# Performance work log

Measured on AMD Instinct MI355X. Metric: run time of the kernel, lower is better.

Reference implementation:

```python
import jax, jax.numpy as jnp
from jax import lax
import numpy as np

B, T, C, V, E, H, OC = 1024, 32, 14, 21128, 200, 50, 8


def gru(x, Wih, Whh, bih, bhh):
    # x: [N, T, E] -> hiddens [N, T, H]; torch nn.GRU gate order (r, z, n)
    Hd = Whh.shape[1]
    xp = jnp.einsum('nte,ge->ntg', x, Wih) + bih  # [N, T, 3H]
    h0 = jnp.zeros((x.shape[0], Hd), x.dtype)

    def step(h, xt):
        gh = h @ Whh.T + bhh
        r = jax.nn.sigmoid(xt[:, :Hd] + gh[:, :Hd])
        z = jax.nn.sigmoid(xt[:, Hd:2 * Hd] + gh[:, Hd:2 * Hd])
        n = jnp.tanh(xt[:, 2 * Hd:] + r * gh[:, 2 * Hd:])
        h_new = (1.0 - z) * n + z * h
        return h_new, h_new

    _, hs = lax.scan(step, h0, jnp.swapaxes(xp, 0, 1))
    return jnp.swapaxes(hs, 0, 1)


def setup_inputs():
    key = jax.random.key(0)
    ks = jax.random.split(key, 32)
    s = 0.1
    inp = {
        'contexts_indices': jax.random.randint(ks[0], (B, T), 0, V),
        'candidates_indices': jax.random.randint(ks[1], (B, C, T), 0, V),
        'y_dev': jax.random.uniform(ks[2], (B, C), dtype=jnp.float32),
        'emb': jax.random.normal(ks[3], (V, E), dtype=jnp.float32),
        'A': jax.random.normal(ks[4], (H, H), dtype=jnp.float32) * s,
        'Wih_c': jax.random.normal(ks[5], (3 * H, E), dtype=jnp.float32) * s,
        'Whh_c': jax.random.normal(ks[6], (3 * H, H), dtype=jnp.float32) * s,
        'bih_c': jnp.zeros((3 * H,), jnp.float32),
        'bhh_c': jnp.zeros((3 * H,), jnp.float32),
        'Wih_r': jax.random.normal(ks[7], (3 * H, E), dtype=jnp.float32) * s,
        'Whh_r': jax.random.normal(ks[8], (3 * H, H), dtype=jnp.float32) * s,
        'bih_r': jnp.zeros((3 * H,), jnp.float32),
        'bhh_r': jnp.zeros((3 * H,), jnp.float32),
        'conv_w': jax.random.normal(ks[9], (OC, 2, 3, 3), dtype=jnp.float32) * s,
        'Wih2': jax.random.normal(ks[10], (3 * H, OC * 10 * 10), dtype=jnp.float32) * s,
        'Whh2': jax.random.normal(ks[11], (3 * H, H), dtype=jnp.float32) * s,
        'bih2': jnp.zeros((3 * H,), jnp.float32),
        'bhh2': jnp.zeros((3 * H,), jnp.float32),
        'fc1_w': jax.random.normal(ks[12], (100, C * H), dtype=jnp.float32) * s,
        'fc1_b': jnp.zeros((100,), jnp.float32),
        'fc2_w': jax.random.normal(ks[13], (C, 100), dtype=jnp.float32) * s,
        'fc2_b': jnp.zeros((C,), jnp.float32),
    }
    return inp


def reference(contexts_indices, candidates_indices, y_dev, emb, A,
              Wih_c, Whh_c, bih_c, bhh_c, Wih_r, Whh_r, bih_r, bhh_r,
              conv_w, Wih2, Whh2, bih2, bhh2, fc1_w, fc1_b, fc2_w, fc2_b):
    b = contexts_indices.shape[0]
    ctx = contexts_indices[:, None, :]                      # [B,1,T]
    ctx_emb = emb[ctx]                                      # [B,1,T,E] (dropout = identity in eval)
    cand_emb = emb[candidates_indices]                      # [B,C,T,E]

    ctx_h = gru(ctx_emb.reshape(-1, T, E), Wih_c, Whh_c, bih_c, bhh_c).reshape(b, 1, T, H)
    cand_h = gru(cand_emb.reshape(-1, T, E), Wih_r, Whh_r, bih_r, bhh_r).reshape(b, C, T, H)

    M1 = jnp.einsum('btph,bcqh->btcpq', ctx_emb, cand_emb)  # [B,1,C,T,T]
    ctx_hA = jnp.einsum('btij,jk->btik', ctx_h, A)
    M2 = jnp.einsum('btph,bcqh->btcpq', ctx_hA, cand_h)

    # faithful to torch: stack on dim 2 then row-major view(-1, 2, T, T)
    M = jnp.stack([M1, M2], axis=2).reshape(-1, 2, T, T)    # [B*C, 2, T, T]

    conv = lax.conv_general_dilated(M, conv_w, (1, 1), 'VALID',
                                    dimension_numbers=('NCHW', 'OIHW', 'NCHW'))  # [B*C, OC, 30, 30]
    pooled = lax.reduce_window(conv, -jnp.inf, lax.max,
                               (1, 1, 3, 3), (1, 1, 3, 3), 'VALID')              # [B*C, OC, 10, 10]

    feats = pooled.reshape(b, C, OC * 10 * 10)              # [B, C, 800]
    Hs = gru(feats, Wih2, Whh2, bih2, bhh2)                 # [B, C, H]
    flat = Hs.reshape(b, -1)                                # [B, C*H]

    hid = jax.nn.relu(flat @ fc1_w.T + fc1_b)
    log_probs = jax.nn.log_softmax(hid @ fc2_w.T + fc2_b, axis=-1)  # softmax then log
    kl = jnp.where(y_dev > 0, y_dev * (jnp.log(y_dev) - log_probs), 0.0)
    return jnp.mean(kl)
```

## Files before the change

kernel.cpp:

```cpp
#include <hip/hip_runtime.h>
#include <math.h>

typedef unsigned short u16;
typedef short s16;
typedef u16 u16x8 __attribute__((ext_vector_type(8)));
typedef s16 short8v __attribute__((ext_vector_type(8)));
typedef float f32x4 __attribute__((ext_vector_type(4)));

__device__ __forceinline__ float b2f(u16 u) {
    return __uint_as_float(((unsigned)u) << 16);
}
__device__ __forceinline__ u16 f2b(float f) {
    unsigned u = __float_as_uint(f);
    unsigned r = (u + 0x7FFFu + ((u >> 16) & 1u)) >> 16;
    return (u16)r;
}

__global__ __launch_bounds__(256) void k_cvt4(
    const float* __restrict__ s0, u16* __restrict__ d0, long n0,
    const float* __restrict__ s1, u16* __restrict__ d1, long n1,
    const float* __restrict__ s2, u16* __restrict__ d2, long n2,
    const float* __restrict__ s3, u16* __restrict__ d3, long n3)
{
    long j = (long)blockIdx.x * 256 + threadIdx.x;
    const float* s; u16* d;
    if (j < n0) { s = s0; d = d0; }
    else {
        j -= n0;
        if (j < n1) { s = s1; d = d1; }
        else {
            j -= n1;
            if (j < n2) { s = s2; d = d2; }
            else {
                j -= n2;
                if (j < n3) { s = s3; d = d3; }
                else return;
            }
        }
    }
    float4 v = ((const float4*)s)[j];
    *(ushort4*)(d + j * 4) = make_ushort4(f2b(v.x), f2b(v.y), f2b(v.z), f2b(v.w));
}

__global__ __launch_bounds__(256) void k_projmm2(
    const u16* __restrict__ embh, const u16* __restrict__ wc,
    const u16* __restrict__ wr, const float* __restrict__ bc,
    const float* __restrict__ br, u16* __restrict__ outc,
    u16* __restrict__ outr, int V)
{
    __shared__ s16 Ab[2048];
    __shared__ s16 Bb[2560];
    __shared__ float bhL[160];
    const int t = threadIdx.x;
    const int w = t >> 6, l = t & 63, lg = l >> 4, lr = l & 15;
    int id = blockIdx.x;
    const int half = (id >= 662) ? 1 : 0;
    id -= half * 662;
    const u16* wh = half ? wr : wc;
    const float* bias = half ? br : bc;
    u16* outp = half ? outr : outc;
    const int mb = id >> 1, nb = id & 1;
    const long rowbase = (long)mb * 64;
    const int colbase = nb * 80;
    if (t < 160) bhL[t] = (t < 150) ? bias[t] : 0.f;

    f32x4 acc[5];
#pragma unroll
    for (int i = 0; i < 5; ++i) acc[i] = (f32x4){0,0,0,0};

    for (int ch = 0; ch < 7; ++ch) {
        __syncthreads();
        {
            int kc = t >> 6, row = t & 63;
            long grow = rowbase + row; if (grow >= V) grow = V - 1;
            int k0 = ch * 32 + kc * 8;
            short8v v = {0,0,0,0,0,0,0,0};
            if (k0 < 200) v = *(const short8v*)(embh + grow * 200 + k0);
            *(short8v*)&Ab[t * 8] = v;
        }
        for (int it = t; it < 320; it += 256) {
            int kc = it / 80, col = it % 80;
            int gcol = colbase + col;
            int k0 = ch * 32 + kc * 8;
            short8v v = {0,0,0,0,0,0,0,0};
            if (gcol < 150 && k0 < 200)
                v = *(const short8v*)(wh + (size_t)gcol * 200 + k0);
            *(short8v*)&Bb[it * 8] = v;
        }
        __syncthreads();
        short8v a = *(short8v*)&Ab[(lg * 64 + w * 16 + lr) * 8];
#pragma unroll
        for (int ct = 0; ct < 5; ++ct) {
            short8v bv = *(short8v*)&Bb[(lg * 80 + ct * 16 + lr) * 8];
            acc[ct] = __builtin_amdgcn_mfma_f32_16x16x32_bf16(a, bv, acc[ct], 0, 0, 0);
        }
    }
#pragma unroll
    for (int ct = 0; ct < 5; ++ct) {
        int gcol = colbase + ct * 16 + lr;
        if (gcol < 150) {
#pragma unroll
            for (int rr = 0; rr < 4; ++rr) {
                long row = rowbase + w * 16 + lg * 4 + rr;
                outp[row * 152 + gcol] = f2b(acc[ct][rr] + bhL[gcol]);
            }
        }
    }
}

template<int MODE, int SEQS>
__device__ __forceinline__ void gru_body(
    const void* __restrict__ xp_, const int* __restrict__ idx,
    const float* __restrict__ Whh, const float* __restrict__ bhh,
    void* __restrict__ hs_, int T, long blk)
{
    __shared__ s16  hbuf[1024];
    __shared__ float ghL[SEQS * 160];
    __shared__ float hL[SEQS * 52];
    __shared__ float bhL[152];
    __shared__ u16 xraw[4864];
    const int t = threadIdx.x;
    const int w = t >> 6, l = t & 63, lg = l >> 4, lr = l & 15;
    constexpr int HST = (MODE == 2) ? 56 : 50;
    constexpr int XROW = SEQS * 152;
    u16*   xbH = xraw;
    float* xbF = (float*)xraw;

    for (int li = t; li < 1024; li += 256) hbuf[li] = 0;
    for (int e = t; e < SEQS * 52; e += 256) hL[e] = 0.f;
    if (t < 152) bhL[t] = (t < 150) ? bhh[t] : 0.f;

    const int te_0 = (w * 3     > 9) ? 9 : w * 3;
    const int te_1 = (w * 3 + 1 > 9) ? 9 : w * 3 + 1;
    const int te_2 = (w * 3 + 2 > 9) ? 9 : w * 3 + 2;
    short8v B00 = {0,0,0,0,0,0,0,0}, B01 = B00, B10 = B00, B11 = B00, B20 = B00, B21 = B00;
    {
        int cols[3] = { te_0 * 16 + lr, te_1 * 16 + lr, te_2 * 16 + lr };
        short8v* frg[6] = { &B00, &B01, &B10, &B11, &B20, &B21 };
#pragma unroll
        for (int ti = 0; ti < 3; ++ti) {
            int col = cols[ti];
            if (col < 150) {
#pragma unroll
                for (int s = 0; s < 2; ++s) {
                    short8v v = {0,0,0,0,0,0,0,0};
#pragma unroll
                    for (int e = 0; e < 8; ++e) {
                        int k = (s * 4 + lg) * 8 + e;
                        if (k < 50) v[e] = (s16)f2b(Whh[col * 50 + k]);
                    }
                    *frg[ti * 2 + s] = v;
                }
            }
        }
    }

    const long seqbase = blk * SEQS;
    const float* xpf = (const float*)xp_;
    const u16*   xph = (const u16*)xp_;
    float* hsf = (float*)hs_;
    u16*   hsh = (u16*)hs_;

    const int rA = (MODE == 2) ? t / 19 : t / 38;
    const int oA = (MODE == 2) ? (t % 19) * 8 : (t % 38) * 4;
    const int rB = (MODE == 2) ? (t + 256) / 19 : (t + 256) / 38;
    const int oB = (MODE == 2) ? ((t + 256) % 19) * 8 : ((t + 256) % 38) * 4;
    const bool actA = (MODE == 2) ? (t < SEQS * 19) : true;
    const bool hasB = (MODE == 2) ? (t + 256 < SEQS * 19) : (t + 256 < SEQS * 38);

    auto rowbase = [&](int rr, int stp) -> size_t {
        long r = seqbase + rr;
        long src = (MODE == 0) ? (r * T + stp) : (long)idx[r * T + stp];
        return (size_t)src * 152;
    };

    if (MODE == 2) {
        if (actA) *(u16x8*)&xbH[rA * 152 + oA] = *(const u16x8*)(xph + rowbase(rA, 0) + oA);
        if (hasB) *(u16x8*)&xbH[rB * 152 + oB] = *(const u16x8*)(xph + rowbase(rB, 0) + oB);
    } else {
        *(float4*)&xbF[rA * 152 + oA] = *(const float4*)(xpf + rowbase(rA, 0) + oA);
        if (hasB)
            *(float4*)&xbF[rB * 152 + oB] = *(const float4*)(xpf + rowbase(rB, 0) + oB);
    }
    __syncthreads();

    for (int st = 0; st < T; ++st) {
        const int cur = st & 1;
        u16x8 pfh0, pfh1;
        float4 pf0, pf1;
        if (st + 1 < T) {
            if (MODE == 2) {
                if (actA) pfh0 = *(const u16x8*)(xph + rowbase(rA, st + 1) + oA);
                if (hasB) pfh1 = *(const u16x8*)(xph + rowbase(rB, st + 1) + oB);
            } else {
                pf0 = *(const float4*)(xpf + rowbase(rA, st + 1) + oA);
                if (hasB) pf1 = *(const float4*)(xpf + rowbase(rB, st + 1) + oB);
            }
        }
        short8v a0 = *(short8v*)&hbuf[((0 + lg) * 16 + lr) * 8];
        short8v a1 = *(short8v*)&hbuf[((4 + lg) * 16 + lr) * 8];
        f32x4 c0 = {0,0,0,0}, c1 = {0,0,0,0}, c2 = {0,0,0,0};
        c0 = __builtin_amdgcn_mfma_f32_16x16x32_bf16(a0, B00, c0, 0, 0, 0);
        c0 = __builtin_amdgcn_mfma_f32_16x16x32_bf16(a1, B01, c0, 0, 0, 0);
        c1 = __builtin_amdgcn_mfma_f32_16x16x32_bf16(a0, B10, c1, 0, 0, 0);
        c1 = __builtin_amdgcn_mfma_f32_16x16x32_bf16(a1, B11, c1, 0, 0, 0);
        c2 = __builtin_amdgcn_mfma_f32_16x16x32_bf16(a0, B20, c2, 0, 0, 0);
        c2 = __builtin_amdgcn_mfma_f32_16x16x32_bf16(a1, B21, c2, 0, 0, 0);
        if (lg * 4 < SEQS) {
            int col0 = te_0 * 16 + lr, col1 = te_1 * 16 + lr, col2 = te_2 * 16 + lr;
            if (col0 < 150) {
#pragma unroll
                for (int r = 0; r < 4; ++r) ghL[(lg * 4 + r) * 160 + col0] = c0[r] + bhL[col0];
            }
            if (col1 < 150) {
#pragma unroll
                for (int r = 0; r < 4; ++r) ghL[(lg * 4 + r) * 160 + col1] = c1[r] + bhL[col1];
            }
            if (col2 < 150) {
#pragma unroll
                for (int r = 0; r < 4; ++r) ghL[(lg * 4 + r) * 160 + col2] = c2[r] + bhL[col2];
            }
        }
        __syncthreads();
        if (st + 1 < T) {
            if (MODE == 2) {
                if (actA) *(u16x8*)&xbH[(cur ^ 1) * XROW + rA * 152 + oA] = pfh0;
                if (hasB) *(u16x8*)&xbH[(cur ^ 1) * XROW + rB * 152 + oB] = pfh1;
            } else {
                *(float4*)&xbF[(cur ^ 1) * XROW + rA * 152 + oA] = pf0;
                if (hasB) *(float4*)&xbF[(cur ^ 1) * XROW + rB * 152 + oB] = pf1;
            }
        }
        for (int item = t; item < SEQS * 50; item += 256) {
            int ss = item / 50, hh = item % 50;
            float xv0, xv1, xv2;
            if (MODE == 2) {
                const u16* xr = &xbH[cur * XROW + ss * 152];
                xv0 = b2f(xr[hh]); xv1 = b2f(xr[50 + hh]); xv2 = b2f(xr[100 + hh]);
            } else {
                const float* xr = &xbF[cur * XROW + ss * 152];
                xv0 = xr[hh]; xv1 = xr[50 + hh]; xv2 = xr[100 + hh];
            }
            float vr  = xv0 + ghL[ss * 160 + hh];
            float vz  = xv1 + ghL[ss * 160 + 50 + hh];
            float ghn = ghL[ss * 160 + 100 + hh];
            float rg = 1.f / (1.f + __expf(-vr));
            float zg = 1.f / (1.f + __expf(-vz));
            float a = xv2 + rg * ghn;
            a = fminf(fmaxf(a, -15.f), 15.f);
            float e2 = __expf(-2.f * a);
            float nn2 = (1.f - e2) / (1.f + e2);
            float hn = (1.f - zg) * nn2 + zg * hL[ss * 52 + hh];
            hL[ss * 52 + hh] = hn;
            hbuf[((hh >> 3) * 16 + ss) * 8 + (hh & 7)] = (s16)f2b(hn);
            size_t ofs = ((size_t)(seqbase + ss) * T + st) * HST + hh;
            if (MODE == 2) hsh[ofs] = f2b(hn); else hsf[ofs] = hn;
        }
        __syncthreads();
    }
}

__global__ __launch_bounds__(256) void k_scan_all(
    const u16* __restrict__ proj_ch, const u16* __restrict__ proj_rh,
    const int* __restrict__ ctx_idx, const int* __restrict__ cand_idx,
    const float* __restrict__ Whh_c, const float* __restrict__ Whh_r,
    const float* __restrict__ bhh_c, const float* __restrict__ bhh_r,
    u16* __restrict__ ctx_hh, u16* __restrict__ candh_h)
{
    const long bid = blockIdx.x;
    const bool cand = (bid < 896);
    gru_body<2, 16>(cand ? (const void*)proj_rh : (const void*)proj_ch,
                    cand ? cand_idx : ctx_idx,
                    cand ? Whh_r : Whh_c,
                    cand ? bhh_r : bhh_c,
                    cand ? (void*)candh_h : (void*)ctx_hh,
                    32, cand ? bid : bid - 896);
}

__global__ __launch_bounds__(256) void k_scan2(
    const float* __restrict__ xp2, const float* __restrict__ Whh2,
    const float* __restrict__ bhh2, float* __restrict__ hs2)
{
    gru_body<0, 8>(xp2, nullptr, Whh2, bhh2, hs2, 14, (long)blockIdx.x);
}

__global__ __launch_bounds__(256) void k_matA(
    const u16* __restrict__ inh, const float* __restrict__ A,
    u16* __restrict__ outh)
{
    __shared__ float AL[50 * 52];
    __shared__ float inL[32 * 52];
    const int t = threadIdx.x;
    for (int e = t; e < 2500; e += 256) AL[(e / 50) * 52 + (e % 50)] = A[e];
    const long rbase = (long)blockIdx.x * 32;
    for (int e = t; e < 1600; e += 256) {
        int r = e / 50, j = e % 50;
        inL[r * 52 + j] = b2f(inh[(rbase + r) * 56 + j]);
    }
    __syncthreads();
    for (int item = t; item < 1600; item += 256) {
        int r = item / 50, kk = item % 50;
        float acc = 0.f;
#pragma unroll 10
        for (int j = 0; j < 50; ++j)
            acc += inL[r * 52 + j] * AL[j * 52 + kk];
        outh[(rbase + r) * 56 + kk] = f2b(acc);
    }
}

__global__ __launch_bounds__(256) void k_matchconv(
    const u16* __restrict__ embh, const int* __restrict__ ctx_idx,
    const int* __restrict__ cand_idx, const u16* __restrict__ ctxA_h,
    const u16* __restrict__ candh_h, const float* __restrict__ conv_w,
    u16* __restrict__ feats, int b0)
{
    __shared__ s16 pool16[9480];
    __shared__ float wL[144];
    __shared__ int ci[32], qi[2][32];
    u16* Mb    = (u16*)pool16;
    u16* convL = (u16*)pool16 + 2184;
    const int t = threadIdx.x;
    const int wg = blockIdx.x;
    const int xcd = wg & 7, q = wg >> 3;
    const int r = q % 14, bq = q / 14;
    const int b = b0 + bq * 8 + xcd;
    const long nl = (long)(bq * 8 + xcd) * 14 + r;
    const int w = t >> 6, l = t & 63, lg = l >> 4, lr = l & 15;

    if (t < 144) wL[t] = conv_w[t];

    f32x4 cacc0 = {0,0,0,0}, cacc1 = {0,0,0,0};
    const int job0 = w * 2, job1 = w * 2 + 1;
    const int ch0 = job0 >> 2, rt0 = (job0 >> 1) & 1, ct0 = job0 & 1;
    const int ch1 = job1 >> 2, rt1 = (job1 >> 1) & 1, ct1 = job1 & 1;

    if (r < 7) {
        const int c0 = 2 * r;
        if (t < 32) ci[t] = ctx_idx[b * 32 + t];
        else if (t < 96)
            qi[(t - 32) >> 5][t & 31] =
                cand_idx[((long)b * 14 + c0 + ((t - 32) >> 5)) * 32 + (t & 31)];
        __syncthreads();
        s16* ctxL = pool16;
        s16* canL = pool16 + 3168;
#pragma unroll
        for (int cnk = 0; cnk < 3; ++cnk) {
            const int kcbase = (cnk == 0) ? 0 : (cnk == 1 ? 12 : 20);
            const int kccnt  = (cnk == 0) ? 12 : 8;
            const int scnt   = (cnk == 0) ? 3 : 2;
            if (cnk) __syncthreads();
            for (int it = t; it < kccnt * 32; it += 256) {
                int kcl = it >> 5, row = it & 31;
                int kc = kcbase + kcl;
                short8v v = {0,0,0,0,0,0,0,0};
                if (kc < 25) v = *(const short8v*)(embh + (size_t)ci[row] * 200 + kc * 8);
                *(short8v*)&ctxL[(kcl * 33 + row) * 8] = v;
            }
            for (int it = t; it < kccnt * 64; it += 256) {
                int kcl = it >> 6, col = it & 63;
                int kc = kcbase + kcl;
                short8v v = {0,0,0,0,0,0,0,0};
                if (kc < 25)
                    v = *(const short8v*)(embh + (size_t)qi[col >> 5][col & 31] * 200 + kc * 8);
                *(short8v*)&canL[(kcl * 65 + col) * 8] = v;
            }
            __syncthreads();
            for (int sl = 0; sl < scnt; ++sl) {
                int kcl = sl * 4 + lg;
                short8v a0 = *(short8v*)&ctxL[(kcl * 33 + rt0 * 16 + lr) * 8];
                short8v b0 = *(short8v*)&canL[(kcl * 65 + ch0 * 32 + ct0 * 16 + lr) * 8];
                short8v b1 = *(short8v*)&canL[(kcl * 65 + ch1 * 32 + ct1 * 16 + lr) * 8];
                cacc0 = __builtin_amdgcn_mfma_f32_16x16x32_bf16(a0, b0, cacc0, 0, 0, 0);
                short8v a1 = (rt0 == rt1) ? a0
                           : *(short8v*)&ctxL[(kcl * 33 + rt1 * 16 + lr) * 8];
                cacc1 = __builtin_amdgcn_mfma_f32_16x16x32_bf16(a1, b1, cacc1, 0, 0, 0);
            }
        }
    } else {
        const int c0 = 2 * (r - 7);
        s16* aL = pool16;
        s16* cL = pool16 + 2112;
        for (int it = t; it < 256; it += 256) {
            int kc = it >> 5, row = it & 31;
            short8v v = {0,0,0,0,0,0,0,0};
            if (kc < 7) {
                v = *(const short8v*)(ctxA_h + (size_t)(b * 32 + row) * 56 + kc * 8);
                if (kc == 6) { v[2] = 0; v[3] = 0; v[4] = 0; v[5] = 0; v[6] = 0; v[7] = 0; }
            }
            *(short8v*)&aL[(kc * 33 + row) * 8] = v;
        }
        for (int it = t; it < 512; it += 256) {
            int kc = it >> 6, col = it & 63;
            long row = ((long)(b - b0) * 14 + c0 + (col >> 5)) * 32 + (col & 31);
            short8v v = {0,0,0,0,0,0,0,0};
            if (kc < 7) {
                v = *(const short8v*)(candh_h + (size_t)row * 56 + kc * 8);
                if (kc == 6) { v[2] = 0; v[3] = 0; v[4] = 0; v[5] = 0; v[6] = 0; v[7] = 0; }
            }
            *(short8v*)&cL[(kc * 65 + col) * 8] = v;
        }
        __syncthreads();
#pragma unroll
        for (int sl = 0; sl < 2; ++sl) {
            int kcl = sl * 4 + lg;
            short8v a0 = *(short8v*)&aL[(kcl * 33 + rt0 * 16 + lr) * 8];
            short8v b0 = *(short8v*)&cL[(kcl * 65 + ch0 * 32 + ct0 * 16 + lr) * 8];
            short8v b1 = *(short8v*)&cL[(kcl * 65 + ch1 * 32 + ct1 * 16 + lr) * 8];
            cacc0 = __builtin_amdgcn_mfma_f32_16x16x32_bf16(a0, b0, cacc0, 0, 0, 0);
            short8v a1 = (rt0 == rt1) ? a0
                       : *(short8v*)&aL[(kcl * 33 + rt1 * 16 + lr) * 8];
            cacc1 = __builtin_amdgcn_mfma_f32_16x16x32_bf16(a1, b1, cacc1, 0, 0, 0);
        }
    }

    __syncthreads();
#pragma unroll
    for (int rr = 0; rr < 4; ++rr) {
        Mb[ch0 * 1092 + (rt0 * 16 + lg * 4 + rr) * 33 + ct0 * 16 + lr] = f2b(cacc0[rr]);
        Mb[ch1 * 1092 + (rt1 * 16 + lg * 4 + rr) * 33 + ct1 * 16 + lr] = f2b(cacc1[rr]);
    }

    short8v Bc = {0,0,0,0,0,0,0,0};
    int dlt[8];
#pragma unroll
    for (int e = 0; e < 8; ++e) {
        int s = lg * 8 + e;
        if (s < 18) {
            int ch = s / 9, r9 = s % 9, ky = r9 / 3, kx = r9 % 3;
            dlt[e] = ch * 1092 + ky * 33 + kx;
            if (lr < 8) Bc[e] = (s16)f2b(wL[lr * 18 + s]);
        } else dlt[e] = 0;
    }
    __syncthreads();

    for (int tile = w; tile < 57; tile += 4) {
        int m = tile * 16 + lr;
        int cy = m / 30, cx = m - cy * 30;
        int base = cy * 33 + cx;
        short8v a;
#pragma unroll
        for (int e = 0; e < 8; ++e) a[e] = (s16)Mb[base + dlt[e]];
        f32x4 c = {0,0,0,0};
        c = __builtin_amdgcn_mfma_f32_16x16x32_bf16(a, Bc, c, 0, 0, 0);
        if (lr < 8) {
#pragma unroll
            for (int rr = 0; rr < 4; ++rr)
                convL[(tile * 16 + lg * 4 + rr) * 8 + lr] = f2b(c[rr]);
        }
    }
    __syncthreads();

    for (int item = t; item < 800; item += 256) {
        int oc = item / 100, rem = item % 100, py = rem / 10, px = rem % 10;
        int m0 = (3 * py) * 30 + 3 * px;
        float mx = -1e30f;
#pragma unroll
        for (int dy = 0; dy < 3; ++dy)
#pragma unroll
            for (int dx = 0; dx < 3; ++dx)
                mx = fmaxf(mx, b2f(convL[(m0 + dy * 30 + dx) * 8 + oc]));
        feats[nl * 800 + item] = f2b(mx);
    }
}

__global__ __launch_bounds__(256) void k_xp2mm(
    const u16* __restrict__ feats, const u16* __restrict__ w2h,
    const float* __restrict__ bih2, float* __restrict__ out)
{
    __shared__ s16 Ab[2048];
    __shared__ s16 Bb[2560];
    __shared__ float bhL[160];
    const int t = threadIdx.x;
    const int w = t >> 6, l = t & 63, lg = l >> 4, lr = l & 15;
    const int mb = blockIdx.x >> 1, nb = blockIdx.x & 1;
    const long rowbase = (long)mb * 64;
    const int colbase = nb * 80;
    if (t < 160) bhL[t] = (t < 150) ? bih2[t] : 0.f;

    f32x4 acc[5];
#pragma unroll
    for (int i = 0; i < 5; ++i) acc[i] = (f32x4){0,0,0,0};

    for (int ch = 0; ch < 25; ++ch) {
        __syncthreads();
        {
            int kc = t >> 6, row = t & 63;
            *(short8v*)&Ab[t * 8] =
                *(const short8v*)(feats + (rowbase + row) * 800 + ch * 32 + kc * 8);
        }
        for (int it = t; it < 320; it += 256) {
            int kc = it / 80, col = it % 80;
            int gcol = colbase + col;
            short8v v = {0,0,0,0,0,0,0,0};
            if (gcol < 150)
                v = *(const short8v*)(w2h + (size_t)gcol * 800 + ch * 32 + kc * 8);
            *(short8v*)&Bb[it * 8] = v;
        }
        __syncthreads();
        short8v a = *(short8v*)&Ab[(lg * 64 + w * 16 + lr) * 8];
#pragma unroll
        for (int ct = 0; ct < 5; ++ct) {
            short8v bv = *(short8v*)&Bb[(lg * 80 + ct * 16 + lr) * 8];
            acc[ct] = __builtin_amdgcn_mfma_f32_16x16x32_bf16(a, bv, acc[ct], 0, 0, 0);
        }
    }
#pragma unroll
    for (int ct = 0; ct < 5; ++ct) {
        int gcol = colbase + ct * 16 + lr;
        if (gcol < 150) {
#pragma unroll
            for (int rr = 0; rr < 4; ++rr) {
                long row = rowbase + w * 16 + lg * 4 + rr;
                out[row * 152 + gcol] = acc[ct][rr] + bhL[gcol];
            }
        }
    }
}

__global__ __launch_bounds__(128) void k_head(
    const float* __restrict__ Hs, const float* __restrict__ w1,
    const float* __restrict__ b1, const float* __restrict__ w2,
    const float* __restrict__ b2, const float* __restrict__ y,
    float* __restrict__ partial)
{
    __shared__ float hr[700];
    __shared__ float hidL[100];
    const int t = threadIdx.x;
    const long b = blockIdx.x;
    for (int e = t; e < 700; e += 128) hr[e] = Hs[b * 700 + e];
    __syncthreads();
    if (t < 100) {
        float acc = b1[t];
        const float4* wp = (const float4*)(w1 + (size_t)t * 700);
        for (int k4 = 0; k4 < 175; ++k4) {
            float4 wv = wp[k4];
            float4 hv = *(float4*)&hr[k4 * 4];
            acc += wv.x * hv.x + wv.y * hv.y + wv.z * hv.z + wv.w * hv.w;
        }
        hidL[t] = fmaxf(acc, 0.f);
    }
    __syncthreads();
    if (t < 64) {
        float logit = -1e30f;
        if (t < 14) {
            logit = b2[t];
            for (int k = 0; k < 100; ++k) logit += hidL[k] * w2[t * 100 + k];
        }
        float m = logit;
        for (int off = 8; off; off >>= 1) m = fmaxf(m, __shfl_xor(m, off, 16));
        float ex = (t < 14) ? __expf(logit - m) : 0.f;
        float se = ex;
        for (int off = 8; off; off >>= 1) se += __shfl_xor(se, off, 16);
        float kl = 0.f;
        if (t < 14) {
            float lp = logit - m - __logf(se);
            float yv = y[b * 14 + t];
            kl = (yv > 0.f) ? yv * (__logf(yv) - lp) : 0.f;
        }
        for (int off = 8; off; off >>= 1) kl += __shfl_xor(kl, off, 16);
        if (t == 0) partial[b] = kl;
    }
}

__global__ __launch_bounds__(256) void k_reduce(
    const float* __restrict__ partial, float* __restrict__ out)
{
    __shared__ float sm[256];
    const int t = threadIdx.x;
    sm[t] = partial[t] + partial[t + 256] + partial[t + 512] + partial[t + 768];
    __syncthreads();
    for (int off = 128; off; off >>= 1) {
        if (t < off) sm[t] += sm[t + off];
        __syncthreads();
    }
    if (t == 0) out[0] = sm[0] * (1.f / 14336.f);
}

extern "C" void kernel_launch(void* const* d_in, const int* in_sizes, int n_in,
                              void* d_out, int out_size, void* d_ws, size_t ws_size,
                              hipStream_t stream)
{
    const int*   ctx_idx  = (const int*)d_in[0];
    const int*   cand_idx = (const int*)d_in[1];
    const float* y_dev    = (const float*)d_in[2];
    const float* emb      = (const float*)d_in[3];
    const float* A        = (const float*)d_in[4];
    const float* Wih_c    = (const float*)d_in[5];
    const float* Whh_c    = (const float*)d_in[6];
    const float* bih_c    = (const float*)d_in[7];
    const float* bhh_c    = (const float*)d_in[8];
    const float* Wih_r    = (const float*)d_in[9];
    const float* Whh_r    = (const float*)d_in[10];
    const float* bih_r    = (const float*)d_in[11];
    const float* bhh_r    = (const float*)d_in[12];
    const float* conv_w   = (const float*)d_in[13];
    const float* Wih2     = (const float*)d_in[14];
    const float* Whh2     = (const float*)d_in[15];
    const float* bih2     = (const float*)d_in[16];
    const float* bhh2     = (const float*)d_in[17];
    const float* fc1_w    = (const float*)d_in[18];
    const float* fc1_b    = (const float*)d_in[19];
    const float* fc2_w    = (const float*)d_in[20];
    const float* fc2_b    = (const float*)d_in[21];

    float* ws = (float*)d_ws;
    u16*   embh    = (u16*)ws;
    u16*   proj_ch = (u16*)(ws + 2112800);
    u16*   proj_rh = (u16*)(ws + 3722784);
    u16*   ctx_hh  = (u16*)(ws + 5332768);
    u16*   ctxA_h  = (u16*)(ws + 6250272);
    u16*   candh_h = (u16*)(ws + 7167776);
    u16*   feats_h = (u16*)(ws + 20012832);
    u16*   w2h     = (u16*)(ws + 25747232);
    u16*   wch     = (u16*)(ws + 25807232);
    u16*   wrh     = (u16*)(ws + 25822232);
    float* xp2     = ws + 25837232;
    float* hs2     = ws + 28016304;
    float* part    = ws + 28733104;

    k_cvt4 <<<4303, 256, 0, stream>>>(emb, embh, 1056400,
                                      Wih2, w2h, 30000,
                                      Wih_c, wch, 7500,
                                      Wih_r, wrh, 7500);
    k_projmm2 <<<1324, 256, 0, stream>>>(embh, wch, wrh, bih_c, bih_r,
                                         proj_ch, proj_rh, 21128);
    k_scan_all <<<960, 256, 0, stream>>>(proj_ch, proj_rh, ctx_idx, cand_idx,
                                         Whh_c, Whh_r, bhh_c, bhh_r,
                                         ctx_hh, candh_h);
    k_matA <<<1024, 256, 0, stream>>>(ctx_hh, A, ctxA_h);
    k_matchconv <<<14336, 256, 0, stream>>>(embh, ctx_idx, cand_idx, ctxA_h, candh_h,
                                            conv_w, feats_h, 0);
    k_xp2mm <<<448, 256, 0, stream>>>(feats_h, w2h, bih2, xp2);
    k_scan2 <<<128, 256, 0, stream>>>(xp2, Whh2, bhh2, hs2);
    k_head <<<1024, 128, 0, stream>>>(hs2, fc1_w, fc1_b, fc2_w, fc2_b, y_dev, part);
    k_reduce <<<1, 256, 0, stream>>>(part, (float*)d_out);
}
```

Before: 330.6 us.

## Run M1 match-conv blocks alongside GRU scans and transpose feats layout

The M1 half of the match/conv work depends only on embeddings, so its blocks now run in the same launch as the context/candidate GRU scans. That fills the GPU while the 960 latency-bound scan blocks execute. The M2 half becomes its own kernel after matA. The pooled features are now stored position-major with 8 channels contiguous, written as vectorized 16-byte stores, and Wih2 is permuted during conversion to match. The mixed kernel carries the larger shared-memory footprint of the scan code for every block, which may lower occupancy for the M1 blocks.

Result: faster. 303.9 us (-8.1%).

```diff
diff --git a/kernel.cpp b/kernel.cpp
--- a/kernel.cpp
+++ b/kernel.cpp
@@ -16,30 +16,36 @@
     return (u16)r;
 }
 
-__global__ __launch_bounds__(256) void k_cvt4(
-    const float* __restrict__ s0, u16* __restrict__ d0, long n0,
-    const float* __restrict__ s1, u16* __restrict__ d1, long n1,
-    const float* __restrict__ s2, u16* __restrict__ d2, long n2,
-    const float* __restrict__ s3, u16* __restrict__ d3, long n3)
+__global__ __launch_bounds__(256) void k_cvt_all(
+    const float* __restrict__ emb, u16* __restrict__ embh,
+    const float* __restrict__ wcf, u16* __restrict__ wch,
+    const float* __restrict__ wrf, u16* __restrict__ wrh,
+    const float* __restrict__ w2f, u16* __restrict__ w2h)
 {
     long j = (long)blockIdx.x * 256 + threadIdx.x;
-    const float* s; u16* d;
-    if (j < n0) { s = s0; d = d0; }
-    else {
-        j -= n0;
-        if (j < n1) { s = s1; d = d1; }
-        else {
-            j -= n1;
-            if (j < n2) { s = s2; d = d2; }
-            else {
-                j -= n2;
-                if (j < n3) { s = s3; d = d3; }
-                else return;
-            }
-        }
-    }
-    float4 v = ((const float4*)s)[j];
-    *(ushort4*)(d + j * 4) = make_ushort4(f2b(v.x), f2b(v.y), f2b(v.z), f2b(v.w));
+    if (j < 1056400) {
+        float4 v = ((const float4*)emb)[j];
+        *(ushort4*)(embh + j * 4) = make_ushort4(f2b(v.x), f2b(v.y), f2b(v.z), f2b(v.w));
+        return;
+    }
+    j -= 1056400;
+    if (j < 7500) {
+        float4 v = ((const float4*)wcf)[j];
+        *(ushort4*)(wch + j * 4) = make_ushort4(f2b(v.x), f2b(v.y), f2b(v.z), f2b(v.w));
+        return;
+    }
+    j -= 7500;
+    if (j < 7500) {
+        float4 v = ((const float4*)wrf)[j];
+        *(ushort4*)(wrh + j * 4) = make_ushort4(f2b(v.x), f2b(v.y), f2b(v.z), f2b(v.w));
+        return;
+    }
+    j -= 7500;
+    if (j < 120000) {
+        int jj = (int)(j / 800), k = (int)(j % 800);
+        int p = k >> 3, oc = k & 7;
+        w2h[jj * 800 + k] = f2b(w2f[jj * 800 + oc * 100 + p]);
+    }
 }
 
 __global__ __launch_bounds__(256) void k_projmm2(
@@ -110,15 +116,15 @@
 
 template<int MODE, int SEQS>
 __device__ __forceinline__ void gru_body(
-    const void* __restrict__ xp_, const int* __restrict__ idx,
+    char* sm, const void* __restrict__ xp_, const int* __restrict__ idx,
     const float* __restrict__ Whh, const float* __restrict__ bhh,
     void* __restrict__ hs_, int T, long blk)
 {
-    __shared__ s16  hbuf[1024];
-    __shared__ float ghL[SEQS * 160];
-    __shared__ float hL[SEQS * 52];
-    __shared__ float bhL[152];
-    __shared__ u16 xraw[4864];
+    s16*   hbuf = (s16*)sm;
+    float* ghL  = (float*)(sm + 2048);
+    float* hL   = (float*)(sm + 2048 + SEQS * 640);
+    float* bhL  = (float*)(sm + 2048 + SEQS * 848);
+    u16*   xraw = (u16*)(sm + 2048 + SEQS * 848 + 608);
     const int t = threadIdx.x;
     const int w = t >> 6, l = t & 63, lg = l >> 4, lr = l & 15;
     constexpr int HST = (MODE == 2) ? 56 : 50;
@@ -260,28 +266,236 @@
     }
 }
 
-__global__ __launch_bounds__(256) void k_scan_all(
+__device__ __forceinline__ void conv_pool_epi(
+    char* sm, u16* __restrict__ feats, long nl, f32x4 cacc0, f32x4 cacc1)
+{
+    s16* pool16 = (s16*)sm;
+    float* wL = (float*)(sm + 18960);
+    u16* Mb    = (u16*)pool16;
+    u16* convL = (u16*)pool16 + 2184;
+    const int t = threadIdx.x;
+    const int w = t >> 6, l = t & 63, lg = l >> 4, lr = l & 15;
+    const int job0 = w * 2, job1 = w * 2 + 1;
+    const int ch0 = job0 >> 2, rt0 = (job0 >> 1) & 1, ct0 = job0 & 1;
+    const int ch1 = job1 >> 2, rt1 = (job1 >> 1) & 1, ct1 = job1 & 1;
+
+    __syncthreads();
+#pragma unroll
+    for (int rr = 0; rr < 4; ++rr) {
+        Mb[ch0 * 1092 + (rt0 * 16 + lg * 4 + rr) * 33 + ct0 * 16 + lr] = f2b(cacc0[rr]);
+        Mb[ch1 * 1092 + (rt1 * 16 + lg * 4 + rr) * 33 + ct1 * 16 + lr] = f2b(cacc1[rr]);
+    }
+
+    short8v Bc = {0,0,0,0,0,0,0,0};
+    int dlt[8];
+#pragma unroll
+    for (int e = 0; e < 8; ++e) {
+        int s = lg * 8 + e;
+        if (s < 18) {
+            int ch = s / 9, r9 = s % 9, ky = r9 / 3, kx = r9 % 3;
+            dlt[e] = ch * 1092 + ky * 33 + kx;
+            if (lr < 8) Bc[e] = (s16)f2b(wL[lr * 18 + s]);
+        } else dlt[e] = 0;
+    }
+    __syncthreads();
+
+    for (int tile = w; tile < 57; tile += 4) {
+        int m = tile * 16 + lr;
+        int cy = m / 30, cx = m - cy * 30;
+        int base = cy * 33 + cx;
+        short8v a;
+#pragma unroll
+        for (int e = 0; e < 8; ++e) a[e] = (s16)Mb[base + dlt[e]];
+        f32x4 c = {0,0,0,0};
+        c = __builtin_amdgcn_mfma_f32_16x16x32_bf16(a, Bc, c, 0, 0, 0);
+        if (lr < 8) {
+#pragma unroll
+            for (int rr = 0; rr < 4; ++rr)
+                convL[(tile * 16 + lg * 4 + rr) * 8 + lr] = f2b(c[rr]);
+        }
+    }
+    __syncthreads();
+
+    if (t < 100) {
+        int py = t / 10, px = t % 10;
+        int m0 = (3 * py) * 30 + 3 * px;
+        float mx[8];
+#pragma unroll
+        for (int c = 0; c < 8; ++c) mx[c] = -1e30f;
+#pragma unroll
+        for (int dy = 0; dy < 3; ++dy)
+#pragma unroll
+            for (int dx = 0; dx < 3; ++dx) {
+                u16x8 v = *(u16x8*)&convL[(m0 + dy * 30 + dx) * 8];
+#pragma unroll
+                for (int c = 0; c < 8; ++c) mx[c] = fmaxf(mx[c], b2f(v[c]));
+            }
+        u16x8 o;
+#pragma unroll
+        for (int c = 0; c < 8; ++c) o[c] = f2b(mx[c]);
+        *(u16x8*)(feats + nl * 800 + t * 8) = o;
+    }
+}
+
+__device__ __forceinline__ void m1_body(
+    char* sm, const u16* __restrict__ embh, const int* __restrict__ ctx_idx,
+    const int* __restrict__ cand_idx, const float* __restrict__ conv_w,
+    u16* __restrict__ feats, int wg)
+{
+    s16* pool16 = (s16*)sm;
+    float* wL = (float*)(sm + 18960);
+    int* ci = (int*)(sm + 19536);
+    int* qi = (int*)(sm + 19664);
+    const int t = threadIdx.x;
+    const int xcd = wg & 7, q = wg >> 3;
+    const int r = q % 7, bq = q / 7;
+    const int b = bq * 8 + xcd;
+    const long nl = (long)b * 14 + r;
+    const int w = t >> 6, l = t & 63, lg = l >> 4, lr = l & 15;
+
+    if (t < 144) wL[t] = conv_w[t];
+
+    f32x4 cacc0 = {0,0,0,0}, cacc1 = {0,0,0,0};
+    const int job0 = w * 2, job1 = w * 2 + 1;
+    const int ch0 = job0 >> 2, rt0 = (job0 >> 1) & 1, ct0 = job0 & 1;
+    const int ch1 = job1 >> 2, rt1 = (job1 >> 1) & 1, ct1 = job1 & 1;
+
+    const int c0 = 2 * r;
+    if (t < 32) ci[t] = ctx_idx[b * 32 + t];
+    else if (t < 96)
+        qi[((t - 32) >> 5) * 32 + (t & 31)] =
+            cand_idx[((long)b * 14 + c0 + ((t - 32) >> 5)) * 32 + (t & 31)];
+    __syncthreads();
+    s16* ctxL = pool16;
+    s16* canL = pool16 + 3168;
+#pragma unroll
+    for (int cnk = 0; cnk < 3; ++cnk) {
+        const int kcbase = (cnk == 0) ? 0 : (cnk == 1 ? 12 : 20);
+        const int kccnt  = (cnk == 0) ? 12 : 8;
+        const int scnt   = (cnk == 0) ? 3 : 2;
+        if (cnk) __syncthreads();
+        for (int it = t; it < kccnt * 32; it += 256) {
+            int kcl = it >> 5, row = it & 31;
+            int kc = kcbase + kcl;
+            short8v v = {0,0,0,0,0,0,0,0};
+            if (kc < 25) v = *(const short8v*)(embh + (size_t)ci[row] * 200 + kc * 8);
+            *(short8v*)&ctxL[(kcl * 33 + row) * 8] = v;
+        }
+        for (int it = t; it < kccnt * 64; it += 256) {
+            int kcl = it >> 6, col = it & 63;
+            int kc = kcbase + kcl;
+            short8v v = {0,0,0,0,0,0,0,0};
+            if (kc < 25)
+                v = *(const short8v*)(embh + (size_t)qi[(col >> 5) * 32 + (col & 31)] * 200 + kc * 8);
+            *(short8v*)&canL[(kcl * 65 + col) * 8] = v;
+        }
+        __syncthreads();
+        for (int sl = 0; sl < scnt; ++sl) {
+            int kcl = sl * 4 + lg;
+            short8v a0 = *(short8v*)&ctxL[(kcl * 33 + rt0 * 16 + lr) * 8];
+            short8v b0 = *(short8v*)&canL[(kcl * 65 + ch0 * 32 + ct0 * 16 + lr) * 8];
+            short8v b1 = *(short8v*)&canL[(kcl * 65 + ch1 * 32 + ct1 * 16 + lr) * 8];
+            cacc0 = __builtin_amdgcn_mfma_f32_16x16x32_bf16(a0, b0, cacc0, 0, 0, 0);
+            short8v a1 = (rt0 == rt1) ? a0
+                       : *(short8v*)&ctxL[(kcl * 33 + rt1 * 16 + lr) * 8];
+            cacc1 = __builtin_amdgcn_mfma_f32_16x16x32_bf16(a1, b1, cacc1, 0, 0, 0);
+        }
+    }
+    conv_pool_epi(sm, feats, nl, cacc0, cacc1);
+}
+
+__global__ __launch_bounds__(256) void k_scan_m1(
     const u16* __restrict__ proj_ch, const u16* __restrict__ proj_rh,
     const int* __restrict__ ctx_idx, const int* __restrict__ cand_idx,
     const float* __restrict__ Whh_c, const float* __restrict__ Whh_r,
     const float* __restrict__ bhh_c, const float* __restrict__ bhh_r,
-    u16* __restrict__ ctx_hh, u16* __restrict__ candh_h)
-{
+    u16* __restrict__ ctx_hh, u16* __restrict__ candh_h,
+    const u16* __restrict__ embh, const float* __restrict__ conv_w,
+    u16* __restrict__ feats)
+{
+    __shared__ long long smq[3244];
+    char* sm = (char*)smq;
     const long bid = blockIdx.x;
-    const bool cand = (bid < 896);
-    gru_body<2, 16>(cand ? (const void*)proj_rh : (const void*)proj_ch,
-                    cand ? cand_idx : ctx_idx,
-                    cand ? Whh_r : Whh_c,
-                    cand ? bhh_r : bhh_c,
-                    cand ? (void*)candh_h : (void*)ctx_hh,
-                    32, cand ? bid : bid - 896);
+    if (bid < 960) {
+        const bool cand = (bid < 896);
+        gru_body<2, 16>(sm,
+                        cand ? (const void*)proj_rh : (const void*)proj_ch,
+                        cand ? cand_idx : ctx_idx,
+                        cand ? Whh_r : Whh_c,
+                        cand ? bhh_r : bhh_c,
+                        cand ? (void*)candh_h : (void*)ctx_hh,
+                        32, cand ? bid : bid - 896);
+    } else {
+        m1_body(sm, embh, ctx_idx, cand_idx, conv_w, feats, (int)(bid - 960));
+    }
+}
+
+__global__ __launch_bounds__(256) void k_m2conv(
+    const u16* __restrict__ ctxA_h, const u16* __restrict__ candh_h,
+    const float* __restrict__ conv_w, u16* __restrict__ feats)
+{
+    __shared__ long long smq[2490];
+    char* sm = (char*)smq;
+    s16* pool16 = (s16*)sm;
+    float* wL = (float*)(sm + 18960);
+    const int t = threadIdx.x;
+    const int wg = blockIdx.x;
+    const int xcd = wg & 7, q = wg >> 3;
+    const int r7 = q % 7, bq = q / 7;
+    const int b = bq * 8 + xcd;
+    const long nl = (long)b * 14 + 7 + r7;
+    const int w = t >> 6, l = t & 63, lg = l >> 4, lr = l & 15;
+
+    if (t < 144) wL[t] = conv_w[t];
+
+    f32x4 cacc0 = {0,0,0,0}, cacc1 = {0,0,0,0};
+    const int job0 = w * 2, job1 = w * 2 + 1;
+    const int ch0 = job0 >> 2, rt0 = (job0 >> 1) & 1, ct0 = job0 & 1;
+    const int ch1 = job1 >> 2, rt1 = (job1 >> 1) & 1, ct1 = job1 & 1;
+
+    const int c0 = 2 * r7;
+    s16* aL = pool16;
+    s16* cL = pool16 + 2112;
+    for (int it = t; it < 256; it += 256) {
+        int kc = it >> 5, row = it & 31;
+        short8v v = {0,0,0,0,0,0,0,0};
+        if (kc < 7) {
+            v = *(const short8v*)(ctxA_h + (size_t)(b * 32 + row) * 56 + kc * 8);
+            if (kc == 6) { v[2] = 0; v[3] = 0; v[4] = 0; v[5] = 0; v[6] = 0; v[7] = 0; }
+        }
+        *(short8v*)&aL[(kc * 33 + row) * 8] = v;
+    }
+    for (int it = t; it < 512; it += 256) {
+        int kc = it >> 6, col = it & 63;
+        long row = ((long)b * 14 + c0 + (col >> 5)) * 32 + (col & 31);
+        short8v v = {0,0,0,0,0,0,0,0};
+        if (kc < 7) {
+            v = *(const short8v*)(candh_h + (size_t)row * 56 + kc * 8);
+            if (kc == 6) { v[2] = 0; v[3] = 0; v[4] = 0; v[5] = 0; v[6] = 0; v[7] = 0; }
+        }
+        *(short8v*)&cL[(kc * 65 + col) * 8] = v;
+    }
+    __syncthreads();
+#pragma unroll
+    for (int sl = 0; sl < 2; ++sl) {
+        int kcl = sl * 4 + lg;
+        short8v a0 = *(short8v*)&aL[(kcl * 33 + rt0 * 16 + lr) * 8];
+        short8v b0 = *(short8v*)&cL[(kcl * 65 + ch0 * 32 + ct0 * 16 + lr) * 8];
+        short8v b1 = *(short8v*)&cL[(kcl * 65 + ch1 * 32 + ct1 * 16 + lr) * 8];
+        cacc0 = __builtin_amdgcn_mfma_f32_16x16x32_bf16(a0, b0, cacc0, 0, 0, 0);
+        short8v a1 = (rt0 == rt1) ? a0
+                   : *(short8v*)&aL[(kcl * 33 + rt1 * 16 + lr) * 8];
+        cacc1 = __builtin_amdgcn_mfma_f32_16x16x32_bf16(a1, b1, cacc1, 0, 0, 0);
+    }
+    conv_pool_epi(sm, feats, nl, cacc0, cacc1);
 }
 
 __global__ __launch_bounds__(256) void k_scan2(
     const float* __restrict__ xp2, const float* __restrict__ Whh2,
     const float* __restrict__ bhh2, float* __restrict__ hs2)
 {
-    gru_body<0, 8>(xp2, nullptr, Whh2, bhh2, hs2, 14, (long)blockIdx.x);
+    __shared__ long long smq[2396];
+    gru_body<0, 8>((char*)smq, xp2, nullptr, Whh2, bhh2, hs2, 14, (long)blockIdx.x);
 }
 
 __global__ __launch_bounds__(256) void k_matA(
@@ -305,161 +519,6 @@
         for (int j = 0; j < 50; ++j)
             acc += inL[r * 52 + j] * AL[j * 52 + kk];
         outh[(rbase + r) * 56 + kk] = f2b(acc);
-    }
-}
-
-__global__ __launch_bounds__(256) void k_matchconv(
-    const u16* __restrict__ embh, const int* __restrict__ ctx_idx,
-    const int* __restrict__ cand_idx, const u16* __restrict__ ctxA_h,
-    const u16* __restrict__ candh_h, const float* __restrict__ conv_w,
-    u16* __restrict__ feats, int b0)
-{
-    __shared__ s16 pool16[9480];
-    __shared__ float wL[144];
-    __shared__ int ci[32], qi[2][32];
-    u16* Mb    = (u16*)pool16;
-    u16* convL = (u16*)pool16 + 2184;
-    const int t = threadIdx.x;
-    const int wg = blockIdx.x;
-    const int xcd = wg & 7, q = wg >> 3;
-    const int r = q % 14, bq = q / 14;
-    const int b = b0 + bq * 8 + xcd;
-    const long nl = (long)(bq * 8 + xcd) * 14 + r;
-    const int w = t >> 6, l = t & 63, lg = l >> 4, lr = l & 15;
-
-    if (t < 144) wL[t] = conv_w[t];
-
-    f32x4 cacc0 = {0,0,0,0}, cacc1 = {0,0,0,0};
-    const int job0 = w * 2, job1 = w * 2 + 1;
-    const int ch0 = job0 >> 2, rt0 = (job0 >> 1) & 1, ct0 = job0 & 1;
-    const int ch1 = job1 >> 2, rt1 = (job1 >> 1) & 1, ct1 = job1 & 1;
-
-    if (r < 7) {
-        const int c0 = 2 * r;
-        if (t < 32) ci[t] = ctx_idx[b * 32 + t];
-        else if (t < 96)
-            qi[(t - 32) >> 5][t & 31] =
-                cand_idx[((long)b * 14 + c0 + ((t - 32) >> 5)) * 32 + (t & 31)];
-        __syncthreads();
-        s16* ctxL = pool16;
-        s16* canL = pool16 + 3168;
-#pragma unroll
-        for (int cnk = 0; cnk < 3; ++cnk) {
-            const int kcbase = (cnk == 0) ? 0 : (cnk == 1 ? 12 : 20);
-            const int kccnt  = (cnk == 0) ? 12 : 8;
-            const int scnt   = (cnk == 0) ? 3 : 2;
-            if (cnk) __syncthreads();
-            for (int it = t; it < kccnt * 32; it += 256) {
-                int kcl = it >> 5, row = it & 31;
-                int kc = kcbase + kcl;
-                short8v v = {0,0,0,0,0,0,0,0};
-                if (kc < 25) v = *(const short8v*)(embh + (size_t)ci[row] * 200 + kc * 8);
-                *(short8v*)&ctxL[(kcl * 33 + row) * 8] = v;
-            }
-            for (int it = t; it < kccnt * 64; it += 256) {
-                int kcl = it >> 6, col = it & 63;
-                int kc = kcbase + kcl;
-                short8v v = {0,0,0,0,0,0,0,0};
-                if (kc < 25)
-                    v = *(const short8v*)(embh + (size_t)qi[col >> 5][col & 31] * 200 + kc * 8);
-                *(short8v*)&canL[(kcl * 65 + col) * 8] = v;
-            }
-            __syncthreads();
-            for (int sl = 0; sl < scnt; ++sl) {
-                int kcl = sl * 4 + lg;
-                short8v a0 = *(short8v*)&ctxL[(kcl * 33 + rt0 * 16 + lr) * 8];
-                short8v b0 = *(short8v*)&canL[(kcl * 65 + ch0 * 32 + ct0 * 16 + lr) * 8];
-                short8v b1 = *(short8v*)&canL[(kcl * 65 + ch1 * 32 + ct1 * 16 + lr) * 8];
-                cacc0 = __builtin_amdgcn_mfma_f32_16x16x32_bf16(a0, b0, cacc0, 0, 0, 0);
-                short8v a1 = (rt0 == rt1) ? a0
-                           : *(short8v*)&ctxL[(kcl * 33 + rt1 * 16 + lr) * 8];
-                cacc1 = __builtin_amdgcn_mfma_f32_16x16x32_bf16(a1, b1, cacc1, 0, 0, 0);
-            }
-        }
-    } else {
-        const int c0 = 2 * (r - 7);
-        s16* aL = pool16;
-        s16* cL = pool16 + 2112;
-        for (int it = t; it < 256; it += 256) {
-            int kc = it >> 5, row = it & 31;
-            short8v v = {0,0,0,0,0,0,0,0};
-            if (kc < 7) {
-                v = *(const short8v*)(ctxA_h + (size_t)(b * 32 + row) * 56 + kc * 8);
-                if (kc == 6) { v[2] = 0; v[3] = 0; v[4] = 0; v[5] = 0; v[6] = 0; v[7] = 0; }
-            }
-            *(short8v*)&aL[(kc * 33 + row) * 8] = v;
-        }
-        for (int it = t; it < 512; it += 256) {
-            int kc = it >> 6, col = it & 63;
-            long row = ((long)(b - b0) * 14 + c0 + (col >> 5)) * 32 + (col & 31);
-            short8v v = {0,0,0,0,0,0,0,0};
-            if (kc < 7) {
-                v = *(const short8v*)(candh_h + (size_t)row * 56 + kc * 8);
-                if (kc == 6) { v[2] = 0; v[3] = 0; v[4] = 0; v[5] = 0; v[6] = 0; v[7] = 0; }
-            }
-            *(short8v*)&cL[(kc * 65 + col) * 8] = v;
-        }
-        __syncthreads();
-#pragma unroll
-        for (int sl = 0; sl < 2; ++sl) {
-            int kcl = sl * 4 + lg;
-            short8v a0 = *(short8v*)&aL[(kcl * 33 + rt0 * 16 + lr) * 8];
-            short8v b0 = *(short8v*)&cL[(kcl * 65 + ch0 * 32 + ct0 * 16 + lr) * 8];
-            short8v b1 = *(short8v*)&cL[(kcl * 65 + ch1 * 32 + ct1 * 16 + lr) * 8];
-            cacc0 = __builtin_amdgcn_mfma_f32_16x16x32_bf16(a0, b0, cacc0, 0, 0, 0);
-            short8v a1 = (rt0 == rt1) ? a0
-                       : *(short8v*)&aL[(kcl * 33 + rt1 * 16 + lr) * 8];
-            cacc1 = __builtin_amdgcn_mfma_f32_16x16x32_bf16(a1, b1, cacc1, 0, 0, 0);
-        }
-    }
-
-    __syncthreads();
-#pragma unroll
-    for (int rr = 0; rr < 4; ++rr) {
-        Mb[ch0 * 1092 + (rt0 * 16 + lg * 4 + rr) * 33 + ct0 * 16 + lr] = f2b(cacc0[rr]);
-        Mb[ch1 * 1092 + (rt1 * 16 + lg * 4 + rr) * 33 + ct1 * 16 + lr] = f2b(cacc1[rr]);
-    }
-
-    short8v Bc = {0,0,0,0,0,0,0,0};
-    int dlt[8];
-#pragma unroll
-    for (int e = 0; e < 8; ++e) {
-        int s = lg * 8 + e;
-        if (s < 18) {
-            int ch = s / 9, r9 = s % 9, ky = r9 / 3, kx = r9 % 3;
-            dlt[e] = ch * 1092 + ky * 33 + kx;
-            if (lr < 8) Bc[e] = (s16)f2b(wL[lr * 18 + s]);
-        } else dlt[e] = 0;
-    }
-    __syncthreads();
-
-    for (int tile = w; tile < 57; tile += 4) {
-        int m = tile * 16 + lr;
-        int cy = m / 30, cx = m - cy * 30;
-        int base = cy * 33 + cx;
-        short8v a;
-#pragma unroll
-        for (int e = 0; e < 8; ++e) a[e] = (s16)Mb[base + dlt[e]];
-        f32x4 c = {0,0,0,0};
-        c = __builtin_amdgcn_mfma_f32_16x16x32_bf16(a, Bc, c, 0, 0, 0);
-        if (lr < 8) {
-#pragma unroll
-            for (int rr = 0; rr < 4; ++rr)
-                convL[(tile * 16 + lg * 4 + rr) * 8 + lr] = f2b(c[rr]);
-        }
-    }
-    __syncthreads();
-
-    for (int item = t; item < 800; item += 256) {
-        int oc = item / 100, rem = item % 100, py = rem / 10, px = rem % 10;
-        int m0 = (3 * py) * 30 + 3 * px;
-        float mx = -1e30f;
-#pragma unroll
-        for (int dy = 0; dy < 3; ++dy)
-#pragma unroll
-            for (int dx = 0; dx < 3; ++dx)
-                mx = fmaxf(mx, b2f(convL[(m0 + dy * 30 + dx) * 8 + oc]));
-        feats[nl * 800 + item] = f2b(mx);
     }
 }
 
@@ -618,18 +677,15 @@
     float* hs2     = ws + 28016304;
     float* part    = ws + 28733104;
 
-    k_cvt4 <<<4303, 256, 0, stream>>>(emb, embh, 1056400,
-                                      Wih2, w2h, 30000,
-                                      Wih_c, wch, 7500,
-                                      Wih_r, wrh, 7500);
+    k_cvt_all <<<4654, 256, 0, stream>>>(emb, embh, Wih_c, wch, Wih_r, wrh,
+                                         Wih2, w2h);
     k_projmm2 <<<1324, 256, 0, stream>>>(embh, wch, wrh, bih_c, bih_r,
                                          proj_ch, proj_rh, 21128);
-    k_scan_all <<<960, 256, 0, stream>>>(proj_ch, proj_rh, ctx_idx, cand_idx,
+    k_scan_m1 <<<8128, 256, 0, stream>>>(proj_ch, proj_rh, ctx_idx, cand_idx,
                                          Whh_c, Whh_r, bhh_c, bhh_r,
-                                         ctx_hh, candh_h);
+                                         ctx_hh, candh_h, embh, conv_w, feats_h);
     k_matA <<<1024, 256, 0, stream>>>(ctx_hh, A, ctxA_h);
-    k_matchconv <<<14336, 256, 0, stream>>>(embh, ctx_idx, cand_idx, ctxA_h, candh_h,
-                                            conv_w, feats_h, 0);
+    k_m2conv <<<7168, 256, 0, stream>>>(ctxA_h, candh_h, conv_w, feats_h);
     k_xp2mm <<<448, 256, 0, stream>>>(feats_h, w2h, bih2, xp2);
     k_scan2 <<<128, 256, 0, stream>>>(xp2, Whh2, bhh2, hs2);
     k_head <<<1024, 128, 0, stream>>>(hs2, fc1_w, fc1_b, fc2_w, fc2_b, y_dev, part);
```
